# Kernel optimization log

Measured on AMD Instinct MI355X. Metric: run time of the kernel, lower is better.

Reference implementation:

```python
import jax, jax.numpy as jnp
import numpy as np

N = 50000
E = 800000
IN_C = 128
HID = 16
HEADS = 8
OUT_C = 64
NEG_SLOPE = 0.2


def setup_inputs() -> dict:
    key = jax.random.key(0)
    ks = jax.random.split(key, 12)
    x = jax.random.normal(ks[0], (N, IN_C), dtype=jnp.float32)
    edge_index = jax.random.randint(ks[1], (2, E), 0, N, dtype=jnp.int32)
    s = 0.1
    W1 = jax.random.normal(ks[2], (IN_C, HEADS * HID), dtype=jnp.float32) * s
    a1_src = jax.random.normal(ks[3], (HEADS, HID), dtype=jnp.float32) * s
    a1_dst = jax.random.normal(ks[4], (HEADS, HID), dtype=jnp.float32) * s
    b1 = jnp.zeros((HEADS * HID,), dtype=jnp.float32)
    W2 = jax.random.normal(ks[5], (HEADS * HID, OUT_C), dtype=jnp.float32) * s
    a2_src = jax.random.normal(ks[6], (1, OUT_C), dtype=jnp.float32) * s
    a2_dst = jax.random.normal(ks[7], (1, OUT_C), dtype=jnp.float32) * s
    b2 = jnp.zeros((OUT_C,), dtype=jnp.float32)
    return {"x": x, "edge_index": edge_index, "W1": W1, "a1_src": a1_src,
            "a1_dst": a1_dst, "b1": b1, "W2": W2, "a2_src": a2_src,
            "a2_dst": a2_dst, "b2": b2}


def gat_conv(x, src, dst, W, a_src, a_dst, b, heads, ch):
    # linear projection -> [N, H, C]
    h = (x @ W).reshape(N, heads, ch)
    # per-node attention logits [N, H]
    al_s = jnp.einsum('nhc,hc->nh', h, a_src)
    al_d = jnp.einsum('nhc,hc->nh', h, a_dst)
    # per-edge logits [E, H]
    e = jax.nn.leaky_relu(al_s[src] + al_d[dst], NEG_SLOPE)
    # segment softmax over incoming edges of each dst node
    emax = jax.ops.segment_max(e, dst, num_segments=N)
    ee = jnp.exp(e - emax[dst])
    denom = jax.ops.segment_sum(ee, dst, num_segments=N)
    alpha = ee / (denom[dst] + 1e-16)
    # weighted scatter-aggregate of source messages
    msg = h[src] * alpha[:, :, None]  # [E, H, C]
    out = jax.ops.segment_sum(msg, dst, num_segments=N)
    return out.reshape(N, heads * ch) + b


def reference(x, edge_index, W1, a1_src, a1_dst, b1, W2, a2_src, a2_dst, b2):
    # add self loops (PyG GATConv default add_self_loops=True)
    loops = jnp.arange(N, dtype=edge_index.dtype)
    src = jnp.concatenate([edge_index[0], loops])
    dst = jnp.concatenate([edge_index[1], loops])
    h = gat_conv(x, src, dst, W1, a1_src, a1_dst, b1, HEADS, HID)
    h = jax.nn.relu(h)
    # dropout p=0.6 is identity in eval mode
    out = gat_conv(h, src, dst, W2, a2_src, a2_dst, b2, 1, OUT_C)
    return out
```

## Files before the change

kernel.cpp:

```cpp
#include <hip/hip_runtime.h>
#include <hip/hip_fp16.h>
#include <math.h>

#define N_NODES 50000
#define E_EDGES 800000
#define IN_C    128
#define HID     16
#define HEADS   8
#define OUT_C   64
#define NEG_SLOPE 0.2f
#define CELLW   64

typedef _Float16 half8 __attribute__((ext_vector_type(8)));
typedef _Float16 half4 __attribute__((ext_vector_type(4)));
typedef float floatx4 __attribute__((ext_vector_type(4)));

__device__ __forceinline__ float lrelu_exp(float v) {
    v = v > 0.f ? v : NEG_SLOPE * v;
    return __expf(v);
}

__global__ __launch_bounds__(256) void fused_gemm_fill(
    const float* __restrict__ X, const float* __restrict__ W, __half* __restrict__ H,
    const float* __restrict__ a_src, const float* __restrict__ a_dst,
    float* __restrict__ als, float* __restrict__ ald,
    const int* __restrict__ src, const int* __restrict__ dst,
    int* __restrict__ cursor, int* __restrict__ ell) {
    __shared__ _Float16 wT[IN_C * 136];
    const int bid = blockIdx.x;
    const int t = threadIdx.x;

    if (bid & 1) {
        const int tid = (bid >> 1) * 256 + t;
        if (tid < E_EDGES / 4) {
            const int4 s4 = ((const int4*)src)[tid];
            const int4 d4 = ((const int4*)dst)[tid];
            const int p0 = atomicAdd(&cursor[d4.x], 1);
            const int p1 = atomicAdd(&cursor[d4.y], 1);
            const int p2 = atomicAdd(&cursor[d4.z], 1);
            const int p3 = atomicAdd(&cursor[d4.w], 1);
            if (p0 < CELLW) __builtin_nontemporal_store(s4.x, &ell[(size_t)d4.x * CELLW + p0]);
            if (p1 < CELLW) __builtin_nontemporal_store(s4.y, &ell[(size_t)d4.y * CELLW + p1]);
            if (p2 < CELLW) __builtin_nontemporal_store(s4.z, &ell[(size_t)d4.z * CELLW + p2]);
            if (p3 < CELLW) __builtin_nontemporal_store(s4.w, &ell[(size_t)d4.w * CELLW + p3]);
        }
        return;
    }

    {
        const int col = t & 127;
        const int kq = (t >> 7) * 4;
        for (int it = 0; it < 16; ++it) {
            const int k0 = it * 8 + kq;
            half4 hv;
            hv[0] = (_Float16)W[(size_t)(k0 + 0) * IN_C + col];
            hv[1] = (_Float16)W[(size_t)(k0 + 1) * IN_C + col];
            hv[2] = (_Float16)W[(size_t)(k0 + 2) * IN_C + col];
            hv[3] = (_Float16)W[(size_t)(k0 + 3) * IN_C + col];
            *(half4*)&wT[col * 136 + k0] = hv;
        }
    }
    __syncthreads();

    const int wave = t >> 6, lane = t & 63;
    const int m = lane & 15, quad = lane >> 4;
    const int r0w = (bid >> 1) * 64 + wave * 16;
    int rl = r0w + m;
    if (rl >= N_NODES) rl = N_NODES - 1;
    const float* Xr = X + (size_t)rl * IN_C;

    floatx4 acc[8];
#pragma unroll
    for (int i = 0; i < 8; ++i) acc[i] = (floatx4){0.f, 0.f, 0.f, 0.f};

#pragma unroll
    for (int kc = 0; kc < 4; ++kc) {
        const int k8 = kc * 32 + quad * 8;
        const float4 xa = *(const float4*)(Xr + k8);
        const float4 xb = *(const float4*)(Xr + k8 + 4);
        half8 a;
        a[0] = (_Float16)xa.x; a[1] = (_Float16)xa.y;
        a[2] = (_Float16)xa.z; a[3] = (_Float16)xa.w;
        a[4] = (_Float16)xb.x; a[5] = (_Float16)xb.y;
        a[6] = (_Float16)xb.z; a[7] = (_Float16)xb.w;
#pragma unroll
        for (int ct = 0; ct < 8; ++ct) {
            const half8 b = *(const half8*)&wT[(ct * 16 + m) * 136 + k8];
            acc[ct] = __builtin_amdgcn_mfma_f32_16x16x32_f16(a, b, acc[ct], 0, 0, 0);
        }
    }

    _Float16* Hh = (_Float16*)H;
#pragma unroll
    for (int ct = 0; ct < 8; ++ct) {
        const float asv = a_src[ct * 16 + m];
        const float adv = a_dst[ct * 16 + m];
#pragma unroll
        for (int r = 0; r < 4; ++r) {
            const int row = r0w + quad * 4 + r;
            const float c = acc[ct][r];
            float ps = c * asv, pd = c * adv;
            ps += __shfl_xor(ps, 1); pd += __shfl_xor(pd, 1);
            ps += __shfl_xor(ps, 2); pd += __shfl_xor(pd, 2);
            ps += __shfl_xor(ps, 4); pd += __shfl_xor(pd, 4);
            ps += __shfl_xor(ps, 8); pd += __shfl_xor(pd, 8);
            if (row < N_NODES) {
                Hh[(size_t)row * IN_C + ct * 16 + m] = (_Float16)c;
                if (m == 0) {
                    als[(size_t)row * HEADS + ct] = ps;
                    ald[(size_t)row * HEADS + ct] = pd;
                }
            }
        }
    }
}

__global__ __launch_bounds__(256) void agg1_gemm2(
    const int* __restrict__ cnt, const int* __restrict__ ell,
    const float* __restrict__ als, const float* __restrict__ ald,
    const __half* __restrict__ H, const float* __restrict__ b,
    const float* __restrict__ W2, const float* __restrict__ a2_src,
    const float* __restrict__ a2_dst, __half* __restrict__ H2,
    float* __restrict__ als2, float* __restrict__ ald2) {
    __shared__ _Float16 w2T[OUT_C * 136];
    __shared__ _Float16 xrowh[32 * 136];
    __shared__ float l2buf[2][32][2];
    const int t = threadIdx.x;

    {
        const int col = t & 63;
        const int kg = t >> 6;
        for (int k0 = kg * 32; k0 < kg * 32 + 32; k0 += 4) {
            half4 hv;
            hv[0] = (_Float16)W2[(size_t)(k0 + 0) * OUT_C + col];
            hv[1] = (_Float16)W2[(size_t)(k0 + 1) * OUT_C + col];
            hv[2] = (_Float16)W2[(size_t)(k0 + 2) * OUT_C + col];
            hv[3] = (_Float16)W2[(size_t)(k0 + 3) * OUT_C + col];
            *(half4*)&w2T[col * 136 + k0] = hv;
        }
    }

    const int nl = t >> 3, h = t & 7;
    int nc = blockIdx.x * 32 + nl;
    if (nc >= N_NODES) nc = N_NODES - 1;
    int deg = cnt[nc];
    deg = deg < CELLW ? deg : CELLW;
    const int* ep = ell + (size_t)nc * CELLW;
    const float ad = ald[nc * HEADS + h];
    float accv[16];
    float ssum;
    {
        const float w = lrelu_exp(als[nc * HEADS + h] + ad);
        const half8* q = (const half8*)(H + ((size_t)nc * HEADS + h) * HID);
        const half8 u0 = q[0], u1 = q[1];
        ssum = w;
#pragma unroll
        for (int j = 0; j < 8; ++j) {
            accv[j] = w * (float)u0[j];
            accv[j + 8] = w * (float)u1[j];
        }
    }
    for (int p = 0; p < deg; p += 4) {
        const int4 s4 = *(const int4*)(ep + p);
        const int s0 = s4.x;
        const int i1 = (p + 1 < deg) ? s4.y : nc;
        const int i2 = (p + 2 < deg) ? s4.z : nc;
        const int i3 = (p + 3 < deg) ? s4.w : nc;
        const float f1 = (p + 1 < deg) ? 1.f : 0.f;
        const float f2 = (p + 2 < deg) ? 1.f : 0.f;
        const float f3 = (p + 3 < deg) ? 1.f : 0.f;
        const float v0 = als[s0 * HEADS + h];
        const float v1 = als[i1 * HEADS + h];
        const float v2 = als[i2 * HEADS + h];
        const float v3 = als[i3 * HEADS + h];
        const half8* q0 = (const half8*)(H + ((size_t)s0 * HEADS + h) * HID);
        const half8* q1 = (const half8*)(H + ((size_t)i1 * HEADS + h) * HID);
        const half8* q2 = (const half8*)(H + ((size_t)i2 * HEADS + h) * HID);
        const half8* q3 = (const half8*)(H + ((size_t)i3 * HEADS + h) * HID);
        const half8 a0 = q0[0], b0 = q0[1];
        const half8 a1 = q1[0], b1 = q1[1];
        const half8 a2 = q2[0], b2 = q2[1];
        const half8 a3 = q3[0], b3 = q3[1];
        const float w0 = lrelu_exp(v0 + ad);
        const float w1 = lrelu_exp(v1 + ad) * f1;
        const float w2 = lrelu_exp(v2 + ad) * f2;
        const float w3 = lrelu_exp(v3 + ad) * f3;
        ssum += (w0 + w1) + (w2 + w3);
#pragma unroll
        for (int j = 0; j < 8; ++j) {
            accv[j]     += w0 * (float)a0[j] + w1 * (float)a1[j] +
                           w2 * (float)a2[j] + w3 * (float)a3[j];
            accv[j + 8] += w0 * (float)b0[j] + w1 * (float)b1[j] +
                           w2 * (float)b2[j] + w3 * (float)b3[j];
        }
    }
    {
        const float inv = 1.f / (ssum + 1e-16f);
        half8 r0, r1;
#pragma unroll
        for (int j = 0; j < 8; ++j) {
            float ra = accv[j] * inv + b[h * 16 + j];
            float rb = accv[j + 8] * inv + b[h * 16 + 8 + j];
            r0[j] = (_Float16)(ra > 0.f ? ra : 0.f);
            r1[j] = (_Float16)(rb > 0.f ? rb : 0.f);
        }
        _Float16* xr = &xrowh[nl * 136 + h * 16];
        *(half8*)(xr) = r0;
        *(half8*)(xr + 8) = r1;
    }

    __syncthreads();

    {
        const int wv = t >> 6, ln = t & 63;
        const int bm = ln & 15, quad = ln >> 4;
        const int mt = wv >> 1;
        const int ntg = wv & 1;
        floatx4 acc0 = (floatx4){0.f, 0.f, 0.f, 0.f};
        floatx4 acc1 = (floatx4){0.f, 0.f, 0.f, 0.f};
        const _Float16* arow  = &xrowh[(mt * 16 + bm) * 136];
        const _Float16* brow0 = &w2T[(ntg * 32 + bm) * 136];
        const _Float16* brow1 = &w2T[(ntg * 32 + 16 + bm) * 136];
#pragma unroll
        for (int kc = 0; kc < 4; ++kc) {
            const int k8 = kc * 32 + quad * 8;
            const half8 a   = *(const half8*)(arow + k8);
            const half8 b0v = *(const half8*)(brow0 + k8);
            const half8 b1v = *(const half8*)(brow1 + k8);
            acc0 = __builtin_amdgcn_mfma_f32_16x16x32_f16(a, b0v, acc0, 0, 0, 0);
            acc1 = __builtin_amdgcn_mfma_f32_16x16x32_f16(a, b1v, acc1, 0, 0, 0);
        }
        const float a2s0 = a2_src[ntg * 32 + bm],      a2d0 = a2_dst[ntg * 32 + bm];
        const float a2s1 = a2_src[ntg * 32 + 16 + bm], a2d1 = a2_dst[ntg * 32 + 16 + bm];
        _Float16* H2h = (_Float16*)H2;
        float psr[4], pdr[4];
#pragma unroll
        for (int r = 0; r < 4; ++r) {
            const float c0 = acc0[r], c1 = acc1[r];
            float ps = c0 * a2s0 + c1 * a2s1;
            float pd = c0 * a2d0 + c1 * a2d1;
            ps += __shfl_xor(ps, 1); pd += __shfl_xor(pd, 1);
            ps += __shfl_xor(ps, 2); pd += __shfl_xor(pd, 2);
            ps += __shfl_xor(ps, 4); pd += __shfl_xor(pd, 4);
            ps += __shfl_xor(ps, 8); pd += __shfl_xor(pd, 8);
            psr[r] = ps; pdr[r] = pd;
            const int row = blockIdx.x * 32 + mt * 16 + quad * 4 + r;
            if (row < N_NODES) {
                H2h[(size_t)row * OUT_C + ntg * 32 + bm] = (_Float16)c0;
                H2h[(size_t)row * OUT_C + ntg * 32 + 16 + bm] = (_Float16)c1;
            }
        }
        if (bm == 0) {
#pragma unroll
            for (int r = 0; r < 4; ++r) {
                l2buf[ntg][mt * 16 + quad * 4 + r][0] = psr[r];
                l2buf[ntg][mt * 16 + quad * 4 + r][1] = pdr[r];
            }
        }
    }
    __syncthreads();
    if (t < 32) {
        const int n2 = blockIdx.x * 32 + t;
        if (n2 < N_NODES) {
            als2[n2] = l2buf[0][t][0] + l2buf[1][t][0];
            ald2[n2] = l2buf[0][t][1] + l2buf[1][t][1];
        }
    }
}

__global__ __launch_bounds__(256) void agg2(
    const int* __restrict__ cnt, const int* __restrict__ ell,
    const float* __restrict__ als, const float* __restrict__ ald,
    const __half* __restrict__ H, const float* __restrict__ b,
    float* __restrict__ out) {
    const int t = threadIdx.x;
    int n = blockIdx.x * 32 + (t >> 3);
    const int j0 = (t & 7) * 8;
    const bool valid = n < N_NODES;
    if (!valid) n = N_NODES - 1;
    int deg = cnt[n];
    deg = deg < CELLW ? deg : CELLW;
    const int* ep = ell + (size_t)n * CELLW;
    const float ad = ald[n];
    float accv[8];
    float ssum;
    {
        const float w = lrelu_exp(als[n] + ad);
        const half8 u = *(const half8*)(H + (size_t)n * OUT_C + j0);
        ssum = w;
#pragma unroll
        for (int k = 0; k < 8; ++k) accv[k] = w * (float)u[k];
    }
    for (int p = 0; p < deg; p += 4) {
        const int4 s4 = *(const int4*)(ep + p);
        const int s0 = s4.x;
        const int i1 = (p + 1 < deg) ? s4.y : n;
        const int i2 = (p + 2 < deg) ? s4.z : n;
        const int i3 = (p + 3 < deg) ? s4.w : n;
        const float f1 = (p + 1 < deg) ? 1.f : 0.f;
        const float f2 = (p + 2 < deg) ? 1.f : 0.f;
        const float f3 = (p + 3 < deg) ? 1.f : 0.f;
        const float v0 = als[s0];
        const float v1 = als[i1];
        const float v2 = als[i2];
        const float v3 = als[i3];
        const half8 u0 = *(const half8*)(H + (size_t)s0 * OUT_C + j0);
        const half8 u1 = *(const half8*)(H + (size_t)i1 * OUT_C + j0);
        const half8 u2 = *(const half8*)(H + (size_t)i2 * OUT_C + j0);
        const half8 u3 = *(const half8*)(H + (size_t)i3 * OUT_C + j0);
        const float w0 = lrelu_exp(v0 + ad);
        const float w1 = lrelu_exp(v1 + ad) * f1;
        const float w2 = lrelu_exp(v2 + ad) * f2;
        const float w3 = lrelu_exp(v3 + ad) * f3;
        ssum += (w0 + w1) + (w2 + w3);
#pragma unroll
        for (int k = 0; k < 8; ++k)
            accv[k] += w0 * (float)u0[k] + w1 * (float)u1[k] +
                       w2 * (float)u2[k] + w3 * (float)u3[k];
    }
    if (valid) {
        const float inv = 1.f / (ssum + 1e-16f);
        floatx4 r0, r1;
        r0[0] = accv[0] * inv + b[j0 + 0]; r0[1] = accv[1] * inv + b[j0 + 1];
        r0[2] = accv[2] * inv + b[j0 + 2]; r0[3] = accv[3] * inv + b[j0 + 3];
        r1[0] = accv[4] * inv + b[j0 + 4]; r1[1] = accv[5] * inv + b[j0 + 5];
        r1[2] = accv[6] * inv + b[j0 + 6]; r1[3] = accv[7] * inv + b[j0 + 7];
        float* op = out + (size_t)n * OUT_C + j0;
        __builtin_nontemporal_store(r0, (floatx4*)op);
        __builtin_nontemporal_store(r1, (floatx4*)(op + 4));
    }
}

extern "C" void kernel_launch(void* const* d_in, const int* in_sizes, int n_in,
                              void* d_out, int out_size, void* d_ws, size_t ws_size,
                              hipStream_t stream) {
    const float* x      = (const float*)d_in[0];
    const int*   ei     = (const int*)d_in[1];
    const float* W1     = (const float*)d_in[2];
    const float* a1_src = (const float*)d_in[3];
    const float* a1_dst = (const float*)d_in[4];
    const float* b1     = (const float*)d_in[5];
    const float* W2     = (const float*)d_in[6];
    const float* a2_src = (const float*)d_in[7];
    const float* a2_dst = (const float*)d_in[8];
    const float* b2     = (const float*)d_in[9];
    const int* src = ei;
    const int* dst = ei + E_EDGES;
    float* outp = (float*)d_out;

    char* wsb = (char*)d_ws;
    __half* h1   = (__half*)wsb;
    __half* h2   = h1 + (size_t)N_NODES * IN_C;
    float*  als1 = (float*)(h2 + (size_t)N_NODES * OUT_C);
    float*  ald1 = als1 + N_NODES * HEADS;
    float*  als2 = ald1 + N_NODES * HEADS;
    float*  ald2 = als2 + N_NODES;
    int*    cursor = (int*)(ald2 + N_NODES);
    int*    ell    = cursor + N_NODES;

    hipMemsetAsync(cursor, 0, N_NODES * sizeof(int), stream);

    {
        const int gemm_blocks = (N_NODES + 63) / 64;
        fused_gemm_fill<<<gemm_blocks * 2, 256, 0, stream>>>(
            x, W1, h1, a1_src, a1_dst, als1, ald1, src, dst, cursor, ell);
    }

    agg1_gemm2<<<(N_NODES + 31) / 32, 256, 0, stream>>>(
        cursor, ell, als1, ald1, h1, b1, W2, a2_src, a2_dst, h2, als2, ald2);

    agg2<<<(N_NODES + 31) / 32, 256, 0, stream>>>(
        cursor, ell, als2, ald2, h2, b2, outp);
}
```

Before: 189.2 us.

## Pre-transpose W1 to fp16 once and stage it into LDS with direct global-to-LDS loads

Adds a prep kernel that zeroes the cursor array and writes a transposed fp16 copy of W1 into workspace, replacing the memset. Each GEMM block then copies that padded W1 image straight into shared memory with global_load_lds instead of doing a strided fp32 read and conversion per block. The X row loads are issued before the barrier so they overlap the LDS fill. This adds one small kernel launch, and the W1t scratch aliases the als2 buffer, which is only safe because als2 is written later.

```diff
diff --git a/kernel.cpp b/kernel.cpp
--- a/kernel.cpp
+++ b/kernel.cpp
@@ -20,8 +20,34 @@
     return __expf(v);
 }
 
+__device__ __forceinline__ void gload_lds16(const void* g, void* l) {
+    __builtin_amdgcn_global_load_lds(
+        (const __attribute__((address_space(1))) void*)g,
+        (__attribute__((address_space(3))) void*)l, 16, 0, 0);
+}
+
+__global__ __launch_bounds__(256) void prep(
+    const float* __restrict__ W1, _Float16* __restrict__ W1t, int* __restrict__ cursor) {
+    const int t = threadIdx.x;
+    const int n = blockIdx.x * 256 + t;
+    if (n < N_NODES) cursor[n] = 0;
+    if (blockIdx.x == 0) {
+        const int col = t & 127;
+        const int kq = (t >> 7) * 4;
+        for (int it = 0; it < 16; ++it) {
+            const int k0 = it * 8 + kq;
+            half4 hv;
+            hv[0] = (_Float16)W1[(size_t)(k0 + 0) * IN_C + col];
+            hv[1] = (_Float16)W1[(size_t)(k0 + 1) * IN_C + col];
+            hv[2] = (_Float16)W1[(size_t)(k0 + 2) * IN_C + col];
+            hv[3] = (_Float16)W1[(size_t)(k0 + 3) * IN_C + col];
+            *(half4*)&W1t[col * 136 + k0] = hv;
+        }
+    }
+}
+
 __global__ __launch_bounds__(256) void fused_gemm_fill(
-    const float* __restrict__ X, const float* __restrict__ W, __half* __restrict__ H,
+    const float* __restrict__ X, const _Float16* __restrict__ W1t, __half* __restrict__ H,
     const float* __restrict__ a_src, const float* __restrict__ a_dst,
     float* __restrict__ als, float* __restrict__ ald,
     const int* __restrict__ src, const int* __restrict__ dst,
@@ -48,19 +74,19 @@
     }
 
     {
-        const int col = t & 127;
-        const int kq = (t >> 7) * 4;
-        for (int it = 0; it < 16; ++it) {
-            const int k0 = it * 8 + kq;
-            half4 hv;
-            hv[0] = (_Float16)W[(size_t)(k0 + 0) * IN_C + col];
-            hv[1] = (_Float16)W[(size_t)(k0 + 1) * IN_C + col];
-            hv[2] = (_Float16)W[(size_t)(k0 + 2) * IN_C + col];
-            hv[3] = (_Float16)W[(size_t)(k0 + 3) * IN_C + col];
-            *(half4*)&wT[col * 136 + k0] = hv;
-        }
-    }
-    __syncthreads();
+        const char* g = (const char*)W1t;
+        char* l = (char*)wT;
+        const int o = t * 16;
+#pragma unroll
+        for (int it = 0; it < 8; ++it) {
+            const int off = it * 4096 + o;
+            gload_lds16(g + off, l + off);
+        }
+        if (t < 128) {
+            const int off = 32768 + o;
+            gload_lds16(g + off, l + off);
+        }
+    }
 
     const int wave = t >> 6, lane = t & 63;
     const int m = lane & 15, quad = lane >> 4;
@@ -69,15 +95,25 @@
     if (rl >= N_NODES) rl = N_NODES - 1;
     const float* Xr = X + (size_t)rl * IN_C;
 
-    floatx4 acc[8];
-#pragma unroll
-    for (int i = 0; i < 8; ++i) acc[i] = (floatx4){0.f, 0.f, 0.f, 0.f};
-
+    float4 xv[8];
 #pragma unroll
     for (int kc = 0; kc < 4; ++kc) {
         const int k8 = kc * 32 + quad * 8;
-        const float4 xa = *(const float4*)(Xr + k8);
-        const float4 xb = *(const float4*)(Xr + k8 + 4);
+        xv[kc * 2]     = *(const float4*)(Xr + k8);
+        xv[kc * 2 + 1] = *(const float4*)(Xr + k8 + 4);
+    }
+
+    __syncthreads();
+
+    floatx4 acc[8];
+#pragma unroll
+    for (int i = 0; i < 8; ++i) acc[i] = (floatx4){0.f, 0.f, 0.f, 0.f};
+
+#pragma unroll
+    for (int kc = 0; kc < 4; ++kc) {
+        const int k8 = kc * 32 + quad * 8;
+        const float4 xa = xv[kc * 2];
+        const float4 xb = xv[kc * 2 + 1];
         half8 a;
         a[0] = (_Float16)xa.x; a[1] = (_Float16)xa.y;
         a[2] = (_Float16)xa.z; a[3] = (_Float16)xa.w;
@@ -358,12 +394,14 @@
     int*    cursor = (int*)(ald2 + N_NODES);
     int*    ell    = cursor + N_NODES;
 
-    hipMemsetAsync(cursor, 0, N_NODES * sizeof(int), stream);
+    _Float16* W1t = (_Float16*)als2;
+
+    prep<<<(N_NODES + 255) / 256, 256, 0, stream>>>(W1, W1t, cursor);
 
     {
         const int gemm_blocks = (N_NODES + 63) / 64;
         fused_gemm_fill<<<gemm_blocks * 2, 256, 0, stream>>>(
-            x, W1, h1, a1_src, a1_dst, als1, ald1, src, dst, cursor, ell);
+            x, W1t, h1, a1_src, a1_dst, als1, ald1, src, dst, cursor, ell);
     }
 
     agg1_gemm2<<<(N_NODES + 31) / 32, 256, 0, stream>>>(
```

New measurement: 192.3 us. About the same (+1.7%).
